# Optimization experiments

Hardware: AMD Instinct MI355X
Metric: run time of the kernel (lower is better)

The kernel has to match this reference:

```python
import jax, jax.numpy as jnp
import numpy as np

H = 1024      # hidden_size (forced by Embedding(1024,1024) concat)
NH = 16       # heads
HD = H // NH  # head_dim = 64
I = 4096      # intermediate_size
V = 1024      # output vocab / embedding rows
T = 4096      # number of timesteps (outer loop)
NSTEPS = 8
EPS = 1e-6
THETA = 10000.0


def rms_norm(x, w):
    var = jnp.mean(x * x, axis=-1, keepdims=True)
    return x * jax.lax.rsqrt(var + EPS) * w


def apply_rope(x, pos):
    # x: [T, NH, L, HD], pos: [L]
    inv_freq = 1.0 / (THETA ** (jnp.arange(0, HD, 2, dtype=jnp.float32) / HD))
    ang = pos.astype(jnp.float32)[:, None] * inv_freq[None, :]  # [L, HD/2]
    cos = jnp.concatenate([jnp.cos(ang), jnp.cos(ang)], axis=-1)  # [L, HD]
    sin = jnp.concatenate([jnp.sin(ang), jnp.sin(ang)], axis=-1)
    x1, x2 = x[..., : HD // 2], x[..., HD // 2 :]
    rot = jnp.concatenate([-x2, x1], axis=-1)
    return x * cos + rot * sin


def decoder_layer(h, Wq, Wk, Wv, Wo, Wg, Wu, Wd, n1, n2):
    # h: [T, L, H]; one Llama decoder layer, called with attention_mask=None
    # (as in the source: layer(current_input, position_ids=arange) -> no causal mask).
    Tb, L, _ = h.shape
    pos = jnp.arange(L)
    x = rms_norm(h, n1)
    q = (x @ Wq).reshape(Tb, L, NH, HD).transpose(0, 2, 1, 3)  # [T,NH,L,HD]
    k = (x @ Wk).reshape(Tb, L, NH, HD).transpose(0, 2, 1, 3)
    v = (x @ Wv).reshape(Tb, L, NH, HD).transpose(0, 2, 1, 3)
    q = apply_rope(q, pos)
    k = apply_rope(k, pos)
    scores = jnp.einsum('thld,thmd->thlm', q, k) / np.sqrt(HD).astype(np.float32)
    attn = jax.nn.softmax(scores, axis=-1)
    ctx = jnp.einsum('thlm,thmd->thld', attn, v)           # [T,NH,L,HD]
    ctx = ctx.transpose(0, 2, 1, 3).reshape(Tb, L, H)
    h = h + ctx @ Wo
    x = rms_norm(h, n2)
    h = h + (jax.nn.silu(x @ Wg) * (x @ Wu)) @ Wd
    return h


def setup_inputs() -> dict:
    key = jax.random.key(0)
    ks = jax.random.split(key, 13)
    s = 0.02
    return {
        'chunk_hidden_states': jax.random.normal(ks[0], (1, T, H), jnp.float32),
        'Wq': jax.random.normal(ks[1], (H, H), jnp.float32) * s,
        'Wk': jax.random.normal(ks[2], (H, H), jnp.float32) * s,
        'Wv': jax.random.normal(ks[3], (H, H), jnp.float32) * s,
        'Wo': jax.random.normal(ks[4], (H, H), jnp.float32) * s,
        'Wg': jax.random.normal(ks[5], (H, I), jnp.float32) * s,
        'Wu': jax.random.normal(ks[6], (H, I), jnp.float32) * s,
        'Wd': jax.random.normal(ks[7], (I, H), jnp.float32) * s,
        'n1': jnp.ones((H,), jnp.float32),
        'n2': jnp.ones((H,), jnp.float32),
        'E': jax.random.normal(ks[8], (V, H), jnp.float32) * s,   # nn.Embedding(1024,1024)
        'Wout': jax.random.normal(ks[9], (H, V), jnp.float32) * s,
        'bout': jnp.zeros((V,), jnp.float32),
    }


def reference(chunk_hidden_states, Wq, Wk, Wv, Wo, Wg, Wu, Wd, n1, n2, E, Wout, bout):
    # The source loops over timesteps sequentially, but each timestep's 8-step
    x0 = chunk_hidden_states[0]                      # [T, H]
    buf = jnp.zeros((T, NSTEPS, H), jnp.float32).at[:, 0].set(x0)
    tokens = []
    for p in range(NSTEPS):                          # fixed 8-step unroll
        h = buf[:, : p + 1]                          # [T, p+1, H]
        out = decoder_layer(h, Wq, Wk, Wv, Wo, Wg, Wu, Wd, n1, n2)
        logits = out[:, -1] @ Wout + bout            # [T, V]
        tok = jnp.argmax(logits, axis=-1)            # argmax of softmax == argmax of logits
        tokens.append(tok)
        if p < NSTEPS - 1:
            buf = buf.at[:, p + 1].set(E[tok])
    return jnp.stack(tokens, axis=-1)                # [T, 8] int tokens
```

## Files before the change

kernel.cpp:

```cpp
#include <hip/hip_runtime.h>
#include <hip/hip_fp16.h>
#include <cmath>

#define Tn 4096
#define Hn 1024
#define NHn 16
#define HDn 64
#define In 4096
#define Vn 1024
#define NSTEPSn 8

enum { EPI_NONE = 0, EPI_ADD = 1, EPI_SILU = 2, EPI_MUL = 3, EPI_BIAS = 4 };

typedef __attribute__((ext_vector_type(8))) _Float16 f16x8;
typedef __attribute__((ext_vector_type(4))) float f32x4;

__device__ inline unsigned short f16rne(float x) {
    return __half_as_ushort(__float2half(x));
}
__device__ inline float f16tof(unsigned short h) {
    return __half2float(__ushort_as_half(h));
}
__device__ inline void split2(float x, unsigned short& h, unsigned short& l) {
    h = f16rne(x);
    float r = (x - f16tof(h)) * 2048.0f;
    l = f16rne(r);
}

__device__ __forceinline__ void gload_lds(const unsigned short* g,
                                          const unsigned short* l) {
    __builtin_amdgcn_global_load_lds(
        (const __attribute__((address_space(1))) unsigned int*)(uintptr_t)g,
        (__attribute__((address_space(3))) unsigned int*)(unsigned int)(uintptr_t)l,
        16, 0, 0);
}

__global__ void rope_tab_kernel(double2* __restrict__ tab) {
    int tid = threadIdx.x;
    int j = tid >> 5, i = tid & 31;
    double inv = exp(-((double)(2 * i) * (1.0 / (double)HDn)) * 9.210340371976184);
    double ang = (double)j * inv;
    double2 cs;
    cs.x = cos(ang);
    cs.y = sin(ang);
    tab[tid] = cs;
}

__global__ __launch_bounds__(256) void presplit_kernel(const float* __restrict__ W,
                                                       unsigned short* __restrict__ W2,
                                                       int K, int N) {
    __shared__ float S[64][65];
    int k0 = blockIdx.y * 64, n0 = blockIdx.x * 64;
    int tid = threadIdx.x;
#pragma unroll
    for (int r = 0; r < 4; r++) {
        int idx = tid + r * 256;
        int kr = idx >> 4, c4 = (idx & 15) << 2;
        float4 v = *(const float4*)(W + (size_t)(k0 + kr) * N + n0 + c4);
        S[kr][c4] = v.x;
        S[kr][c4 + 1] = v.y;
        S[kr][c4 + 2] = v.z;
        S[kr][c4 + 3] = v.w;
    }
    __syncthreads();
    size_t PS = (size_t)N * K;
#pragma unroll
    for (int r = 0; r < 4; r++) {
        int idx = tid + r * 256;
        int kq = idx & 15, n = idx >> 4;
        ushort4 hq, lq;
        split2(S[4 * kq + 0][n], hq.x, lq.x);
        split2(S[4 * kq + 1][n], hq.y, lq.y);
        split2(S[4 * kq + 2][n], hq.z, lq.z);
        split2(S[4 * kq + 3][n], hq.w, lq.w);
        size_t off = (size_t)(n0 + n) * K + k0 + 4 * kq;
        *(ushort4*)(W2 + off) = hq;
        *(ushort4*)(W2 + PS + off) = lq;
    }
}

__global__ __launch_bounds__(256) void rmsnorm2_kernel(const float* __restrict__ x,
                                                       const float* __restrict__ w,
                                                       unsigned short* __restrict__ y2,
                                                       size_t stride) {
    int t = blockIdx.x;
    const float4* xr = (const float4*)(x + (size_t)t * Hn);
    float4 v = xr[threadIdx.x];
    double ss = (double)v.x * v.x + (double)v.y * v.y + (double)v.z * v.z + (double)v.w * v.w;
#pragma unroll
    for (int o = 1; o < 64; o <<= 1) ss += __shfl_xor(ss, o, 64);
    __shared__ double red[4];
    if ((threadIdx.x & 63) == 0) red[threadIdx.x >> 6] = ss;
    __syncthreads();
    double tot = red[0] + red[1] + red[2] + red[3];
    double rs = 1.0 / sqrt(tot * (1.0 / Hn) + 1e-6);
    const float4* wr = (const float4*)w;
    float4 wv = wr[threadIdx.x];
    float o[4];
    o[0] = (float)((double)v.x * rs * (double)wv.x);
    o[1] = (float)((double)v.y * rs * (double)wv.y);
    o[2] = (float)((double)v.z * rs * (double)wv.z);
    o[3] = (float)((double)v.w * rs * (double)wv.w);
    ushort4 hq, lq;
    split2(o[0], hq.x, lq.x);
    split2(o[1], hq.y, lq.y);
    split2(o[2], hq.z, lq.z);
    split2(o[3], hq.w, lq.w);
    size_t off = (size_t)t * Hn + threadIdx.x * 4;
    *(ushort4*)(y2 + off) = hq;
    *(ushort4*)(y2 + stride + off) = lq;
}

__global__ __launch_bounds__(256) void attn_kernel(const float* __restrict__ q,
                                                   const float* __restrict__ K0,
                                                   const float* __restrict__ V0,
                                                   const float* __restrict__ EK,
                                                   const float* __restrict__ EV,
                                                   const int* __restrict__ toks,
                                                   const double2* __restrict__ tab,
                                                   unsigned short* __restrict__ ctx2,
                                                   size_t stride, int p) {
    int wv = blockIdx.x * 4 + (threadIdx.x >> 6);
    int lane = threadIdx.x & 63;
    int g = lane >> 3, s = lane & 7;
    int pair = wv * 8 + g;
    int t = pair >> 4;
    int head = pair & 15;
    int colbase = pair << 6;

    double qv[8], qr[8];
#pragma unroll
    for (int k = 0; k < 8; k++) qv[k] = (double)q[colbase + s + 8 * k];
#pragma unroll
    for (int k = 0; k < 4; k++) {
        double2 cs = tab[p * 32 + s + 8 * k];
        qr[k] = qv[k] * cs.x - qv[k + 4] * cs.y;
        qr[k + 4] = qv[k + 4] * cs.x + qv[k] * cs.y;
    }

    double sc[NSTEPSn];
    int tk[NSTEPSn];
    double m = -1e300;
    for (int j = 0; j <= p; j++) {
        double kr[8];
        if (j == 0) {
            tk[0] = 0;
#pragma unroll
            for (int k = 0; k < 8; k++) kr[k] = (double)K0[colbase + s + 8 * k];
        } else {
            int tok = toks[(size_t)t * NSTEPSn + (j - 1)];
            tk[j] = tok;
            size_t eb = (size_t)tok * Hn + (head << 6);
            double kv[8];
#pragma unroll
            for (int k = 0; k < 8; k++) kv[k] = (double)EK[eb + s + 8 * k];
#pragma unroll
            for (int k = 0; k < 4; k++) {
                double2 cs = tab[j * 32 + s + 8 * k];
                kr[k] = kv[k] * cs.x - kv[k + 4] * cs.y;
                kr[k + 4] = kv[k + 4] * cs.x + kv[k] * cs.y;
            }
        }
        double pr = 0.0;
#pragma unroll
        for (int k = 0; k < 8; k++) pr += qr[k] * kr[k];
#pragma unroll
        for (int o = 1; o < 8; o <<= 1) pr += __shfl_xor(pr, o, 64);
        sc[j] = pr * 0.125;
        m = fmax(m, sc[j]);
    }

    double den = 0.0;
    for (int j = 0; j <= p; j++) {
        sc[j] = (double)expf((float)(sc[j] - m));
        den += sc[j];
    }
    double invd = 1.0 / den;

    double acc[8];
#pragma unroll
    for (int k = 0; k < 8; k++) acc[k] = 0.0;
    for (int j = 0; j <= p; j++) {
        if (j == 0) {
#pragma unroll
            for (int k = 0; k < 8; k++)
                acc[k] += sc[0] * (double)V0[colbase + s + 8 * k];
        } else {
            size_t eb = (size_t)tk[j] * Hn + (head << 6);
#pragma unroll
            for (int k = 0; k < 8; k++)
                acc[k] += sc[j] * (double)EV[eb + s + 8 * k];
        }
    }

#pragma unroll
    for (int k = 0; k < 8; k++) {
        unsigned short h, l;
        split2((float)(acc[k] * invd), h, l);
        ctx2[colbase + s + 8 * k] = h;
        ctx2[stride + colbase + s + 8 * k] = l;
    }
}

#define BUFU 12288
template <int EPI, bool PAIR>
__global__ __launch_bounds__(512, 4) void gemm2_kernel(
    const unsigned short* __restrict__ A2, size_t strideA,
    const unsigned short* __restrict__ B2, size_t strideB, int ldbk,
    float* Cf, unsigned short* C2, size_t strideC,
    const float* aux, int K, int ldc) {
    __shared__ __align__(16) unsigned short lds[3 * BUFU];

    int tid = threadIdx.x;
    int wv = tid >> 6, lane = tid & 63;
    int wr = wv >> 2;
    int wc = wv & 3;

    int f = blockIdx.x;
    int xcd = f & 7;
    int j = f >> 3;
    int bmPer = gridDim.x >> 6;
    int mblk = (xcd * bmPer + (j >> 3)) * 64;
    int nblk = (j & 7) * 128;

    int rsel = lane >> 2;
    int csel = ((lane & 3) ^ ((lane >> 2) & 3)) << 3;
    const unsigned short* gseg[3];
    unsigned lseg[3];
#pragma unroll
    for (int i = 0; i < 3; i++) {
        int s = wv * 3 + i;
        if (s < 8) {
            int pl = s >> 2, sub = s & 3;
            gseg[i] = A2 + (size_t)pl * strideA +
                      (size_t)(mblk + sub * 16 + rsel) * K + csel;
            lseg[i] = pl * 2048 + sub * 512;
        } else {
            int u = s - 8;
            int pl = u >> 3, sub = u & 7;
            gseg[i] = B2 + (size_t)pl * strideB +
                      (size_t)(nblk + sub * 16 + rsel) * ldbk + csel;
            lseg[i] = 4096 + pl * 4096 + sub * 512;
        }
    }

    f32x4 acc[2][2], accl[2][2];
    double accd[2][2][4];
#pragma unroll
    for (int mt = 0; mt < 2; mt++)
#pragma unroll
        for (int nt = 0; nt < 2; nt++) {
            acc[mt][nt] = (f32x4){0.f, 0.f, 0.f, 0.f};
            accl[mt][nt] = (f32x4){0.f, 0.f, 0.f, 0.f};
#pragma unroll
            for (int r = 0; r < 4; r++) accd[mt][nt][r] = 0.0;
        }

    int rA = lane & 15;
    unsigned fo = (rA << 5) + (((lane >> 4) ^ (lane & 3)) << 3);

    int nc = K >> 5;

#pragma unroll
    for (int i = 0; i < 3; i++) gload_lds(gseg[i], lds + lseg[i]);
#pragma unroll
    for (int i = 0; i < 3; i++) gload_lds(gseg[i] + 32, lds + BUFU + lseg[i]);
    asm volatile("s_waitcnt vmcnt(3)" ::: "memory");
    __builtin_amdgcn_s_barrier();

    f16x8 Ah[2], Al[2], Bh[2], Bl[2];
#pragma unroll
    for (int mt = 0; mt < 2; mt++)
        Ah[mt] = *(const f16x8*)(lds + (wr * 2 + mt) * 512 + fo);
#pragma unroll
    for (int nt = 0; nt < 2; nt++)
        Bh[nt] = *(const f16x8*)(lds + 4096 + (wc * 2 + nt) * 512 + fo);

    int rd = 0, w2 = 2;
    for (int c = 0; c < nc; ++c) {
        const unsigned short* Ar = lds + rd * BUFU;
        unsigned short* Lw = lds + w2 * BUFU;
        const bool pf = (c + 2 < nc);
        const bool nx = (c + 1 < nc);
        int koff = (c + 2) << 5;

        if (pf) {
            gload_lds(gseg[0] + koff, Lw + lseg[0]);
            gload_lds(gseg[1] + koff, Lw + lseg[1]);
        }
        if (c > 0 && (c & 1) == 0) {
#pragma unroll
            for (int mt = 0; mt < 2; mt++)
#pragma unroll
                for (int nt = 0; nt < 2; nt++)
#pragma unroll
                    for (int r = 0; r < 4; r++) {
                        accd[mt][nt][r] += (double)acc[mt][nt][r] +
                                           (double)accl[mt][nt][r] * 4.8828125e-4;
                        acc[mt][nt][r] = 0.f;
                        accl[mt][nt][r] = 0.f;
                    }
        }
        __builtin_amdgcn_s_barrier();
#pragma unroll
        for (int nt = 0; nt < 2; nt++)
            Bl[nt] = *(const f16x8*)(Ar + 8192 + (wc * 2 + nt) * 512 + fo);
        __builtin_amdgcn_s_setprio(1);
#pragma unroll
        for (int mt = 0; mt < 2; mt++)
#pragma unroll
            for (int nt = 0; nt < 2; nt++)
                acc[mt][nt] = __builtin_amdgcn_mfma_f32_16x16x32_f16(
                    Ah[mt], Bh[nt], acc[mt][nt], 0, 0, 0);
        __builtin_amdgcn_s_setprio(0);
        __builtin_amdgcn_s_barrier();

        if (pf) {
            gload_lds(gseg[2] + koff, Lw + lseg[2]);
        }
        __builtin_amdgcn_s_barrier();
#pragma unroll
        for (int mt = 0; mt < 2; mt++)
            Al[mt] = *(const f16x8*)(Ar + 2048 + (wr * 2 + mt) * 512 + fo);
        __builtin_amdgcn_s_setprio(1);
#pragma unroll
        for (int mt = 0; mt < 2; mt++)
#pragma unroll
            for (int nt = 0; nt < 2; nt++)
                accl[mt][nt] = __builtin_amdgcn_mfma_f32_16x16x32_f16(
                    Ah[mt], Bl[nt], accl[mt][nt], 0, 0, 0);
        __builtin_amdgcn_s_setprio(0);
        __builtin_amdgcn_s_barrier();

        if (nx) {
            if (pf)
                asm volatile("s_waitcnt vmcnt(3)" ::: "memory");
            else
                asm volatile("s_waitcnt vmcnt(0)" ::: "memory");
        }
        __builtin_amdgcn_s_barrier();
        __builtin_amdgcn_s_setprio(1);
#pragma unroll
        for (int mt = 0; mt < 2; mt++)
#pragma unroll
            for (int nt = 0; nt < 2; nt++)
                accl[mt][nt] = __builtin_amdgcn_mfma_f32_16x16x32_f16(
                    Al[mt], Bh[nt], accl[mt][nt], 0, 0, 0);
        __builtin_amdgcn_s_setprio(0);
        if (nx) {
            int rdn = (rd + 1 == 3) ? 0 : rd + 1;
            const unsigned short* An = lds + rdn * BUFU;
#pragma unroll
            for (int mt = 0; mt < 2; mt++)
                Ah[mt] = *(const f16x8*)(An + (wr * 2 + mt) * 512 + fo);
#pragma unroll
            for (int nt = 0; nt < 2; nt++)
                Bh[nt] = *(const f16x8*)(An + 4096 + (wc * 2 + nt) * 512 + fo);
        }
        __builtin_amdgcn_s_barrier();

        rd = (rd + 1 == 3) ? 0 : rd + 1;
        w2 = (w2 + 1 == 3) ? 0 : w2 + 1;
    }

#pragma unroll
    for (int mt = 0; mt < 2; mt++)
#pragma unroll
        for (int nt = 0; nt < 2; nt++)
#pragma unroll
            for (int r = 0; r < 4; r++)
                accd[mt][nt][r] += (double)acc[mt][nt][r] +
                                   (double)accl[mt][nt][r] * 4.8828125e-4;

#pragma unroll
    for (int mt = 0; mt < 2; mt++)
#pragma unroll
        for (int nt = 0; nt < 2; nt++) {
            int n = nblk + wc * 32 + nt * 16 + (lane & 15);
            int mb = mblk + wr * 32 + mt * 16 + ((lane >> 4) << 2);
#pragma unroll
            for (int r = 0; r < 4; r++) {
                int m = mb + r;
                size_t off = (size_t)m * ldc + n;
                double v = accd[mt][nt][r];
                if (EPI == EPI_ADD) v += (double)aux[off];
                if (EPI == EPI_SILU) {
                    float vf = (float)v;
                    v = (double)(vf / (1.0f + expf(-vf)));
                }
                if (EPI == EPI_MUL) v *= (double)aux[off];
                if (EPI == EPI_BIAS) v += (double)aux[n];
                if (PAIR) {
                    unsigned short h, l;
                    split2((float)v, h, l);
                    C2[off] = h;
                    C2[strideC + off] = l;
                } else {
                    Cf[off] = (float)v;
                }
            }
        }
}

__global__ __launch_bounds__(256) void argmax_kernel(const float* __restrict__ logits,
                                                     int* __restrict__ out_tok, int p) {
    int t = blockIdx.x;
    const float* lr = logits + (size_t)t * Vn;
    float bv = -INFINITY;
    int bi = 0x7fffffff;
    for (int j = threadIdx.x; j < Vn; j += 256) {
        float v = lr[j];
        if (v > bv || (v == bv && j < bi)) {
            bv = v;
            bi = j;
        }
    }
#pragma unroll
    for (int o = 1; o < 64; o <<= 1) {
        float ov = __shfl_xor(bv, o, 64);
        int oi = __shfl_xor(bi, o, 64);
        if (ov > bv || (ov == bv && oi < bi)) {
            bv = ov;
            bi = oi;
        }
    }
    __shared__ float sv[4];
    __shared__ int si[4];
    if ((threadIdx.x & 63) == 0) {
        sv[threadIdx.x >> 6] = bv;
        si[threadIdx.x >> 6] = bi;
    }
    __syncthreads();
    if (threadIdx.x == 0) {
        for (int w = 1; w < 4; w++) {
            if (sv[w] > bv || (sv[w] == bv && si[w] < bi)) {
                bv = sv[w];
                bi = si[w];
            }
        }
        out_tok[(size_t)t * NSTEPSn + p] = bi;
    }
}

__global__ __launch_bounds__(256) void embed_kernel(const float* __restrict__ E,
                                                    const int* __restrict__ toks,
                                                    float* __restrict__ x, int p) {
    int t = blockIdx.x;
    int tok = toks[(size_t)t * NSTEPSn + p];
    float4 v = ((const float4*)(E + (size_t)tok * Hn))[threadIdx.x];
    ((float4*)(x + (size_t)t * Hn))[threadIdx.x] = v;
}

extern "C" void kernel_launch(void* const* d_in, const int* in_sizes, int n_in,
                              void* d_out, int out_size, void* d_ws, size_t ws_size,
                              hipStream_t stream) {
    const float* x0 = (const float*)d_in[0];
    const float* Wq = (const float*)d_in[1];
    const float* Wk = (const float*)d_in[2];
    const float* Wv = (const float*)d_in[3];
    const float* Wo = (const float*)d_in[4];
    const float* Wg = (const float*)d_in[5];
    const float* Wu = (const float*)d_in[6];
    const float* Wd = (const float*)d_in[7];
    const float* n1 = (const float*)d_in[8];
    const float* n2 = (const float*)d_in[9];
    const float* Emb = (const float*)d_in[10];
    const float* Wout = (const float*)d_in[11];
    const float* bout = (const float*)d_in[12];
    int* toks = (int*)d_out;

    float* ws = (float*)d_ws;
    const size_t M1 = 1024 * 1024;
    float* EK = ws;
    float* EV = ws + 1 * M1;
    float* K0 = ws + 2 * M1;
    float* V0 = ws + 6 * M1;
    float* xb = ws + 10 * M1;
    float* qb = ws + 14 * M1;
    float* Gc = ws + 18 * M1;
    unsigned short* s2a = (unsigned short*)(ws + 22 * M1);
    unsigned short* s2g = (unsigned short*)(ws + 28 * M1);
    double2* tab = (double2*)(ws + 34 * M1);
    unsigned short* W2q = (unsigned short*)(ws + 34 * M1 + 1024);
    unsigned short* W2k = W2q + 3 * M1;
    unsigned short* W2v = W2k + 3 * M1;
    unsigned short* W2o = W2v + 3 * M1;
    unsigned short* W2t = W2o + 3 * M1;
    unsigned short* W2g = W2t + 3 * M1;
    unsigned short* W2u = W2g + 12 * M1;
    unsigned short* W2d = W2u + 12 * M1;

    const size_t STH = (size_t)Tn * Hn;
    const size_t SVH = (size_t)Vn * Hn;
    const size_t SW1 = M1;
    const size_t SW4 = 4 * M1;

    dim3 blk(256);
    dim3 gblk(512);
    const int gTH = 512;
    const int gVH = 128;
    const int gAT = (Tn * NHn) / 32;

    rope_tab_kernel<<<1, 256, 0, stream>>>(tab);
    presplit_kernel<<<dim3(16, 16), blk, 0, stream>>>(Wq, W2q, Hn, Hn);
    presplit_kernel<<<dim3(16, 16), blk, 0, stream>>>(Wk, W2k, Hn, Hn);
    presplit_kernel<<<dim3(16, 16), blk, 0, stream>>>(Wv, W2v, Hn, Hn);
    presplit_kernel<<<dim3(16, 16), blk, 0, stream>>>(Wo, W2o, Hn, Hn);
    presplit_kernel<<<dim3(16, 16), blk, 0, stream>>>(Wout, W2t, Hn, Vn);
    presplit_kernel<<<dim3(In / 64, Hn / 64), blk, 0, stream>>>(Wg, W2g, Hn, In);
    presplit_kernel<<<dim3(In / 64, Hn / 64), blk, 0, stream>>>(Wu, W2u, Hn, In);
    presplit_kernel<<<dim3(Hn / 64, In / 64), blk, 0, stream>>>(Wd, W2d, In, Hn);
    rmsnorm2_kernel<<<Vn, 256, 0, stream>>>(Emb, n1, s2a, SVH);
    gemm2_kernel<EPI_NONE, false><<<gVH, gblk, 0, stream>>>(
        s2a, SVH, W2k, SW1, Hn, EK, nullptr, 0, nullptr, Hn, Hn);
    gemm2_kernel<EPI_NONE, false><<<gVH, gblk, 0, stream>>>(
        s2a, SVH, W2v, SW1, Hn, EV, nullptr, 0, nullptr, Hn, Hn);

    for (int p = 0; p < NSTEPSn; p++) {
        const float* src = (p == 0) ? x0 : xb;

        rmsnorm2_kernel<<<Tn, 256, 0, stream>>>(src, n1, s2a, STH);
        gemm2_kernel<EPI_NONE, false><<<gTH, gblk, 0, stream>>>(
            s2a, STH, W2q, SW1, Hn, qb, nullptr, 0, nullptr, Hn, Hn);
        if (p == 0) {
            gemm2_kernel<EPI_NONE, false><<<gTH, gblk, 0, stream>>>(
                s2a, STH, W2k, SW1, Hn, K0, nullptr, 0, nullptr, Hn, Hn);
            gemm2_kernel<EPI_NONE, false><<<gTH, gblk, 0, stream>>>(
                s2a, STH, W2v, SW1, Hn, V0, nullptr, 0, nullptr, Hn, Hn);
        }
        attn_kernel<<<gAT, 256, 0, stream>>>(qb, K0, V0, EK, EV, toks,
                                             tab, s2a, STH, p);
        gemm2_kernel<EPI_ADD, false><<<gTH, gblk, 0, stream>>>(
            s2a, STH, W2o, SW1, Hn, xb, nullptr, 0, src, Hn, Hn);
        rmsnorm2_kernel<<<Tn, 256, 0, stream>>>(xb, n2, s2a, STH);
        for (int c = 0; c < 4; c++) {
            gemm2_kernel<EPI_SILU, false><<<gTH, gblk, 0, stream>>>(
                s2a, STH, W2g + (size_t)c * M1, SW4, Hn,
                Gc, nullptr, 0, nullptr, Hn, 1024);
            gemm2_kernel<EPI_MUL, true><<<gTH, gblk, 0, stream>>>(
                s2a, STH, W2u + (size_t)c * M1, SW4, Hn,
                nullptr, s2g, STH, Gc, Hn, 1024);
            if (c < 3) {
                gemm2_kernel<EPI_ADD, false><<<gTH, gblk, 0, stream>>>(
                    s2g, STH, W2d + (size_t)c * 1024, SW4, In,
                    qb, nullptr, 0, (c == 0) ? xb : qb, Hn, Hn);
            } else {
                gemm2_kernel<EPI_ADD, true><<<gTH, gblk, 0, stream>>>(
                    s2g, STH, W2d + (size_t)c * 1024, SW4, In,
                    nullptr, s2a, STH, qb, Hn, Hn);
            }
        }
        gemm2_kernel<EPI_BIAS, false><<<gTH, gblk, 0, stream>>>(
            s2a, STH, W2t, SW1, Hn, qb, nullptr, 0, bout, Hn, Vn);
        argmax_kernel<<<Tn, 256, 0, stream>>>(qb, toks, p);
        if (p < NSTEPSn - 1) embed_kernel<<<Tn, 256, 0, stream>>>(Emb, toks, xb, p);
    }
}
```

Baseline: 5.804 ms.

## Collapse split-f16 GEMM main loop to one barrier and change LDS swizzle

The K-loop of the split-precision (hi/lo f16) MFMA GEMM is restructured. All three global-to-LDS prefetches are issued together at the top of each iteration, and all A/B hi/lo fragments are then read from LDS. The 12 MFMAs run as one prioritized burst, and a single barrier per iteration replaces the previous five. Register-level prefetch of the next chunk's fragments is removed. The XOR swizzle used on LDS writes and reads is changed to key on row>>1 instead of row, to alter the bank-conflict pattern. The goal is to cut barrier stalls, at the cost of LDS-read latency that is no longer overlapped with compute.

```diff
diff --git a/kernel.cpp b/kernel.cpp
--- a/kernel.cpp
+++ b/kernel.cpp
@@ -224,7 +224,7 @@
     int nblk = (j & 7) * 128;
 
     int rsel = lane >> 2;
-    int csel = ((lane & 3) ^ ((lane >> 2) & 3)) << 3;
+    int csel = ((lane & 3) ^ ((lane >> 3) & 3)) << 3;
     const unsigned short* gseg[3];
     unsigned lseg[3];
 #pragma unroll
@@ -257,7 +257,7 @@
         }
 
     int rA = lane & 15;
-    unsigned fo = (rA << 5) + (((lane >> 4) ^ (lane & 3)) << 3);
+    unsigned fo = (rA << 5) + ((((lane >> 4) ^ ((lane >> 1) & 3))) << 3);
 
     int nc = K >> 5;
 
@@ -267,14 +267,6 @@
     for (int i = 0; i < 3; i++) gload_lds(gseg[i] + 32, lds + BUFU + lseg[i]);
     asm volatile("s_waitcnt vmcnt(3)" ::: "memory");
     __builtin_amdgcn_s_barrier();
-
-    f16x8 Ah[2], Al[2], Bh[2], Bl[2];
-#pragma unroll
-    for (int mt = 0; mt < 2; mt++)
-        Ah[mt] = *(const f16x8*)(lds + (wr * 2 + mt) * 512 + fo);
-#pragma unroll
-    for (int nt = 0; nt < 2; nt++)
-        Bh[nt] = *(const f16x8*)(lds + 4096 + (wc * 2 + nt) * 512 + fo);
 
     int rd = 0, w2 = 2;
     for (int c = 0; c < nc; ++c) {
@@ -287,7 +279,21 @@
         if (pf) {
             gload_lds(gseg[0] + koff, Lw + lseg[0]);
             gload_lds(gseg[1] + koff, Lw + lseg[1]);
-        }
+            gload_lds(gseg[2] + koff, Lw + lseg[2]);
+        }
+
+        f16x8 Ah[2], Al[2], Bh[2], Bl[2];
+#pragma unroll
+        for (int mt = 0; mt < 2; mt++) {
+            Ah[mt] = *(const f16x8*)(Ar + (wr * 2 + mt) * 512 + fo);
+            Al[mt] = *(const f16x8*)(Ar + 2048 + (wr * 2 + mt) * 512 + fo);
+        }
+#pragma unroll
+        for (int nt = 0; nt < 2; nt++) {
+            Bh[nt] = *(const f16x8*)(Ar + 4096 + (wc * 2 + nt) * 512 + fo);
+            Bl[nt] = *(const f16x8*)(Ar + 8192 + (wc * 2 + nt) * 512 + fo);
+        }
+
         if (c > 0 && (c & 1) == 0) {
 #pragma unroll
             for (int mt = 0; mt < 2; mt++)
@@ -301,10 +307,7 @@
                         accl[mt][nt][r] = 0.f;
                     }
         }
-        __builtin_amdgcn_s_barrier();
-#pragma unroll
-        for (int nt = 0; nt < 2; nt++)
-            Bl[nt] = *(const f16x8*)(Ar + 8192 + (wc * 2 + nt) * 512 + fo);
+
         __builtin_amdgcn_s_setprio(1);
 #pragma unroll
         for (int mt = 0; mt < 2; mt++)
@@ -312,50 +315,25 @@
             for (int nt = 0; nt < 2; nt++)
                 acc[mt][nt] = __builtin_amdgcn_mfma_f32_16x16x32_f16(
                     Ah[mt], Bh[nt], acc[mt][nt], 0, 0, 0);
-        __builtin_amdgcn_s_setprio(0);
-        __builtin_amdgcn_s_barrier();
-
-        if (pf) {
-            gload_lds(gseg[2] + koff, Lw + lseg[2]);
-        }
-        __builtin_amdgcn_s_barrier();
-#pragma unroll
-        for (int mt = 0; mt < 2; mt++)
-            Al[mt] = *(const f16x8*)(Ar + 2048 + (wr * 2 + mt) * 512 + fo);
-        __builtin_amdgcn_s_setprio(1);
 #pragma unroll
         for (int mt = 0; mt < 2; mt++)
 #pragma unroll
             for (int nt = 0; nt < 2; nt++)
                 accl[mt][nt] = __builtin_amdgcn_mfma_f32_16x16x32_f16(
                     Ah[mt], Bl[nt], accl[mt][nt], 0, 0, 0);
+#pragma unroll
+        for (int mt = 0; mt < 2; mt++)
+#pragma unroll
+            for (int nt = 0; nt < 2; nt++)
+                accl[mt][nt] = __builtin_amdgcn_mfma_f32_16x16x32_f16(
+                    Al[mt], Bh[nt], accl[mt][nt], 0, 0, 0);
         __builtin_amdgcn_s_setprio(0);
-        __builtin_amdgcn_s_barrier();
 
         if (nx) {
             if (pf)
                 asm volatile("s_waitcnt vmcnt(3)" ::: "memory");
             else
                 asm volatile("s_waitcnt vmcnt(0)" ::: "memory");
-        }
-        __builtin_amdgcn_s_barrier();
-        __builtin_amdgcn_s_setprio(1);
-#pragma unroll
-        for (int mt = 0; mt < 2; mt++)
-#pragma unroll
-            for (int nt = 0; nt < 2; nt++)
-                accl[mt][nt] = __builtin_amdgcn_mfma_f32_16x16x32_f16(
-                    Al[mt], Bh[nt], accl[mt][nt], 0, 0, 0);
-        __builtin_amdgcn_s_setprio(0);
-        if (nx) {
-            int rdn = (rd + 1 == 3) ? 0 : rd + 1;
-            const unsigned short* An = lds + rdn * BUFU;
-#pragma unroll
-            for (int mt = 0; mt < 2; mt++)
-                Ah[mt] = *(const f16x8*)(An + (wr * 2 + mt) * 512 + fo);
-#pragma unroll
-            for (int nt = 0; nt < 2; nt++)
-                Bh[nt] = *(const f16x8*)(An + 4096 + (wc * 2 + nt) * 512 + fo);
         }
         __builtin_amdgcn_s_barrier();
 
```

New measurement: 5.606 ms. 3.4% less time.
